# Kernel optimization log

Hardware: AMD Instinct MI355X
Metric: run time of the kernel (lower is better)

The kernel has to match this reference:

```python
import jax, jax.numpy as jnp
import numpy as np

N, E = 50000, 600000
IN_DIM, H, D = 256, 4, 128
NEG_SLOPE = 0.2


def setup_inputs() -> dict:
    key = jax.random.key(0)
    ks = jax.random.split(key, 9)
    x = jax.random.normal(ks[0], (N, IN_DIM), dtype=jnp.float32)
    src = jax.random.randint(ks[1], (E,), 0, N, dtype=jnp.int32)
    dst = jax.random.randint(ks[2], (E,), 0, N, dtype=jnp.int32)
    # layer 0: in=256 -> H*D=512; layer 1: in=H*D=512 -> H*D=512
    s0 = 1.0 / np.sqrt(IN_DIM)
    s1 = 1.0 / np.sqrt(H * D)
    W0 = jax.random.normal(ks[3], (IN_DIM, H * D), dtype=jnp.float32) * s0
    al0 = jax.random.normal(ks[4], (H, D), dtype=jnp.float32) * s1
    ar0 = jax.random.normal(ks[5], (H, D), dtype=jnp.float32) * s1
    W1 = jax.random.normal(ks[6], (H * D, H * D), dtype=jnp.float32) * s1
    al1 = jax.random.normal(ks[7], (H, D), dtype=jnp.float32) * s1
    ar1 = jax.random.normal(ks[8], (H, D), dtype=jnp.float32) * s1
    return {"x": x, "src": src, "dst": dst,
            "W0": W0, "al0": al0, "ar0": ar0,
            "W1": W1, "al1": al1, "ar1": ar1}


def gat_conv(x, W, al, ar, src, dst):
    """One DGL-style GATConv layer. x:[N,in] -> out:[N,H,D] (post relu)."""
    h = (x @ W).reshape(N, H, D)                       # fc, no bias
    el = jnp.sum(h * al, axis=-1)                      # [N,H]
    er = jnp.sum(h * ar, axis=-1)                      # [N,H]
    e = jax.nn.leaky_relu(el[src] + er[dst], NEG_SLOPE)  # [E,H]
    # edge softmax over incoming edges of each dst node (numerically stable)
    m = jax.ops.segment_max(e, dst, num_segments=N)    # [N,H]
    m = jnp.where(jnp.isfinite(m), m, 0.0)             # empty segments -> -inf
    ex = jnp.exp(e - m[dst])                           # [E,H]
    denom = jax.ops.segment_sum(ex, dst, num_segments=N)  # [N,H]
    alpha = ex / denom[dst]                            # [E,H]
    msg = alpha[:, :, None] * h[src]                   # [E,H,D]
    rst = jax.ops.segment_sum(msg, dst, num_segments=N)  # [N,H,D]
    return jax.nn.relu(rst)                            # activation=F.relu


def reference(x, src, dst, W0, al0, ar0, W1, al1, ar1):
    h = gat_conv(x, W0, al0, ar0, src, dst)            # [N,H,D]
    h = h.reshape(N, H * D)                            # flatten(1)
    h = gat_conv(h, W1, al1, ar1, src, dst)            # [N,H,D]
    return h.mean(axis=1)                              # mean over heads -> [N,D]
```

## Files before the change

kernel.cpp:

```cpp
#include <hip/hip_runtime.h>

#define NN 50000
#define NE 600000
#define DD 128
#define HD 512
#define NB 196

typedef unsigned short u16;
typedef __attribute__((ext_vector_type(8))) short short8;
typedef __attribute__((ext_vector_type(4))) float floatx4;

__device__ inline float b2f(u16 u) {
  return __uint_as_float(((unsigned int)u) << 16);
}
__device__ inline u16 f2b(float f) {
  unsigned int u = __float_as_uint(f);
  u = u + 0x7FFFu + ((u >> 16) & 1u);
  return (u16)(u >> 16);
}

__global__ void transpose_k(const float* __restrict__ W, u16* __restrict__ Wt, int K) {
  int idx = blockIdx.x * 256 + threadIdx.x;
  if (idx >= K * 512) return;
  int k = idx >> 9, n = idx & 511;
  Wt[n * K + k] = f2b(W[idx]);
}

__global__ void count_k(const int* __restrict__ dst, int* __restrict__ counts) {
  int e = blockIdx.x * 256 + threadIdx.x;
  if (e < NE) atomicAdd(&counts[dst[e]], 1);
}

__global__ __launch_bounds__(256) void blockscan_k(const int* __restrict__ counts,
                                                   int* __restrict__ rowp,
                                                   int* __restrict__ bsums) {
  __shared__ int tmp[256];
  int t = threadIdx.x;
  int i = blockIdx.x * 256 + t;
  int v = (i < NN) ? counts[i] : 0;
  tmp[t] = v;
  __syncthreads();
  for (int off = 1; off < 256; off <<= 1) {
    int u = (t >= off) ? tmp[t - off] : 0;
    __syncthreads();
    tmp[t] += u;
    __syncthreads();
  }
  if (i < NN) rowp[i] = tmp[t] - v;
  if (t == 255) bsums[blockIdx.x] = tmp[t];
}

__global__ __launch_bounds__(256) void bscan_k(const int* __restrict__ bsums,
                                               int* __restrict__ boffs) {
  __shared__ int tmp[256];
  int t = threadIdx.x;
  int v = (t < NB) ? bsums[t] : 0;
  tmp[t] = v;
  __syncthreads();
  for (int off = 1; off < 256; off <<= 1) {
    int u = (t >= off) ? tmp[t - off] : 0;
    __syncthreads();
    tmp[t] += u;
    __syncthreads();
  }
  if (t < NB) boffs[t] = tmp[t] - v;
}

__global__ void addoff_k(int* __restrict__ rowp, int* __restrict__ cursor,
                         const int* __restrict__ boffs) {
  int i = blockIdx.x * 256 + threadIdx.x;
  if (i < NN) {
    int v = rowp[i] + boffs[blockIdx.x];
    rowp[i] = v;
    cursor[i] = v;
  }
  if (i == 0) rowp[NN] = NE;
}

__global__ void scatter_k(const int* __restrict__ src, const int* __restrict__ dst,
                          int* __restrict__ cursor, int* __restrict__ csrs) {
  int e = blockIdx.x * 256 + threadIdx.x;
  if (e < NE) {
    int d = dst[e];
    int pos = atomicAdd(&cursor[d], 1);
    csrs[pos] = src[e];
  }
}

template <int K, bool A_F32>
__global__ __launch_bounds__(256) void gemm_el_er(
    const void* __restrict__ Ap, const u16* __restrict__ Wt,
    const float* __restrict__ al, const float* __restrict__ ar,
    u16* __restrict__ h, float* __restrict__ el, float* __restrict__ er) {
  constexpr int WS = 40;
  __shared__ u16 Wt_s[512 * WS];

  const int tid = threadIdx.x;
  const int w = tid >> 6, lane = tid & 63, quad = lane >> 4, l16 = lane & 15;
  const int rg = w >> 1, cg = w & 1;
  const int bm = blockIdx.x;

  floatx4 acc[16] = {};

  const int rowA = bm * 32 + rg * 16 + l16;
  const long arow = (rowA < NN) ? rowA : (NN - 1);

  const int sr0 = tid >> 2;
  const int sck = (tid & 3) * 8;

  for (int k0 = 0; k0 < K; k0 += 32) {
#pragma unroll
    for (int rr = 0; rr < 8; ++rr) {
      int r = sr0 + rr * 64;
      *(short8*)(Wt_s + r * WS + sck) =
          *(const short8*)(Wt + (long)r * K + k0 + sck);
    }
    __syncthreads();
    short8 af;
    if (A_F32) {
      const float* Af = (const float*)Ap;
      floatx4 v0 = *(const floatx4*)(Af + arow * K + k0 + quad * 8);
      floatx4 v1 = *(const floatx4*)(Af + arow * K + k0 + quad * 8 + 4);
      u16 tmp[8];
#pragma unroll
      for (int j = 0; j < 4; ++j) tmp[j] = f2b(v0[j]);
#pragma unroll
      for (int j = 0; j < 4; ++j) tmp[4 + j] = f2b(v1[j]);
      af = *(short8*)tmp;
    } else {
      af = *(const short8*)((const u16*)Ap + arow * K + k0 + quad * 8);
    }
#pragma unroll
    for (int ct = 0; ct < 16; ++ct) {
      short8 bf = *(const short8*)(Wt_s + (cg * 256 + ct * 16 + l16) * WS + quad * 8);
      acc[ct] = __builtin_amdgcn_mfma_f32_16x16x32_bf16(af, bf, acc[ct], 0, 0, 0);
    }
    __syncthreads();
  }

  float alv[16], arv[16];
#pragma unroll
  for (int ct = 0; ct < 16; ++ct) {
    int col = cg * 256 + ct * 16 + l16;
    alv[ct] = al[col];
    arv[ct] = ar[col];
  }
#pragma unroll
  for (int reg = 0; reg < 4; ++reg) {
    const int r = bm * 32 + rg * 16 + quad * 4 + reg;
    float pel[2] = {0.f, 0.f}, per_[2] = {0.f, 0.f};
#pragma unroll
    for (int ct = 0; ct < 16; ++ct) {
      int hh = ct >> 3;
      float v = acc[ct][reg];
      pel[hh] += v * alv[ct];
      per_[hh] += v * arv[ct];
    }
#pragma unroll
    for (int m = 1; m < 16; m <<= 1) {
      pel[0] += __shfl_xor(pel[0], m, 64);
      pel[1] += __shfl_xor(pel[1], m, 64);
      per_[0] += __shfl_xor(per_[0], m, 64);
      per_[1] += __shfl_xor(per_[1], m, 64);
    }
    if (r < NN) {
#pragma unroll
      for (int ct = 0; ct < 16; ++ct)
        h[(long)r * HD + cg * 256 + ct * 16 + l16] = f2b(acc[ct][reg]);
      if (l16 == 0) {
        el[r * 4 + cg * 2] = pel[0];
        el[r * 4 + cg * 2 + 1] = pel[1];
        er[r * 4 + cg * 2] = per_[0];
        er[r * 4 + cg * 2 + 1] = per_[1];
      }
    }
  }
}

template <int MODE>
__global__ __launch_bounds__(256) void aggregate(
    const u16* __restrict__ h, const float* __restrict__ el,
    const float* __restrict__ er, const int* __restrict__ rowp,
    const int* __restrict__ csrs, u16* __restrict__ ob, float* __restrict__ of) {
  const int wv = threadIdx.x >> 6, lane = threadIdx.x & 63;
  const int n = blockIdx.x * 4 + wv;
  if (n >= NN) return;
  const int base = rowp[n];
  const int deg = rowp[n + 1] - base;
  const int head = lane >> 4;

  if (deg == 0) {
    if (MODE == 0) {
      short8 z = {};
      *(short8*)(ob + (long)n * HD + lane * 8) = z;
    } else if (lane < 16) {
      floatx4 z = {};
      *(floatx4*)(of + (long)n * DD + lane * 8) = z;
      *(floatx4*)(of + (long)n * DD + lane * 8 + 4) = z;
    }
    return;
  }

  const floatx4 erv = *(const floatx4*)(er + n * 4);

  float mx[4] = {-1e30f, -1e30f, -1e30f, -1e30f};
  for (int i = lane; i < deg; i += 64) {
    int s = csrs[base + i];
    const floatx4 ev = *(const floatx4*)(el + s * 4);
#pragma unroll
    for (int hh = 0; hh < 4; ++hh) {
      float e = ev[hh] + erv[hh];
      e = (e > 0.f) ? e : 0.2f * e;
      mx[hh] = fmaxf(mx[hh], e);
    }
  }
#pragma unroll
  for (int hh = 0; hh < 4; ++hh)
#pragma unroll
    for (int m = 1; m < 64; m <<= 1) mx[hh] = fmaxf(mx[hh], __shfl_xor(mx[hh], m, 64));

  float sm[4] = {0.f, 0.f, 0.f, 0.f};
  for (int i = lane; i < deg; i += 64) {
    int s = csrs[base + i];
    const floatx4 ev = *(const floatx4*)(el + s * 4);
#pragma unroll
    for (int hh = 0; hh < 4; ++hh) {
      float e = ev[hh] + erv[hh];
      e = (e > 0.f) ? e : 0.2f * e;
      sm[hh] += __expf(e - mx[hh]);
    }
  }
#pragma unroll
  for (int hh = 0; hh < 4; ++hh)
#pragma unroll
    for (int m = 1; m < 64; m <<= 1) sm[hh] += __shfl_xor(sm[hh], m, 64);

  const float m_h = mx[head];
  const float inv_h = 1.f / sm[head];
  const float er_h = erv[head];

  float acc[8] = {0.f, 0.f, 0.f, 0.f, 0.f, 0.f, 0.f, 0.f};
  int i = 0;
  for (; i + 4 <= deg; i += 4) {
    int s0 = csrs[base + i], s1 = csrs[base + i + 1];
    int s2 = csrs[base + i + 2], s3 = csrs[base + i + 3];
    const short8 hv0 = *(const short8*)(h + (long)s0 * HD + lane * 8);
    const short8 hv1 = *(const short8*)(h + (long)s1 * HD + lane * 8);
    const short8 hv2 = *(const short8*)(h + (long)s2 * HD + lane * 8);
    const short8 hv3 = *(const short8*)(h + (long)s3 * HD + lane * 8);
    float e0 = el[s0 * 4 + head] + er_h;
    float e1 = el[s1 * 4 + head] + er_h;
    float e2 = el[s2 * 4 + head] + er_h;
    float e3 = el[s3 * 4 + head] + er_h;
    e0 = (e0 > 0.f) ? e0 : 0.2f * e0;
    e1 = (e1 > 0.f) ? e1 : 0.2f * e1;
    e2 = (e2 > 0.f) ? e2 : 0.2f * e2;
    e3 = (e3 > 0.f) ? e3 : 0.2f * e3;
    float w0 = __expf(e0 - m_h) * inv_h;
    float w1 = __expf(e1 - m_h) * inv_h;
    float w2 = __expf(e2 - m_h) * inv_h;
    float w3 = __expf(e3 - m_h) * inv_h;
#pragma unroll
    for (int j = 0; j < 8; ++j) acc[j] += w0 * b2f((u16)hv0[j]);
#pragma unroll
    for (int j = 0; j < 8; ++j) acc[j] += w1 * b2f((u16)hv1[j]);
#pragma unroll
    for (int j = 0; j < 8; ++j) acc[j] += w2 * b2f((u16)hv2[j]);
#pragma unroll
    for (int j = 0; j < 8; ++j) acc[j] += w3 * b2f((u16)hv3[j]);
  }
  for (; i < deg; ++i) {
    int s = csrs[base + i];
    float e = el[s * 4 + head] + er_h;
    const short8 hv = *(const short8*)(h + (long)s * HD + lane * 8);
    e = (e > 0.f) ? e : 0.2f * e;
    float wgt = __expf(e - m_h) * inv_h;
#pragma unroll
    for (int j = 0; j < 8; ++j) acc[j] += wgt * b2f((u16)hv[j]);
  }

#pragma unroll
  for (int j = 0; j < 8; ++j) acc[j] = fmaxf(acc[j], 0.f);

  if (MODE == 0) {
    u16 ub[8];
#pragma unroll
    for (int j = 0; j < 8; ++j) ub[j] = f2b(acc[j]);
    *(short8*)(ob + (long)n * HD + lane * 8) = *(short8*)ub;
  } else {
#pragma unroll
    for (int j = 0; j < 8; ++j) acc[j] += __shfl_xor(acc[j], 16, 64);
#pragma unroll
    for (int j = 0; j < 8; ++j) acc[j] += __shfl_xor(acc[j], 32, 64);
    if (lane < 16) {
      floatx4 o0, o1;
#pragma unroll
      for (int j = 0; j < 4; ++j) o0[j] = acc[j] * 0.25f;
#pragma unroll
      for (int j = 0; j < 4; ++j) o1[j] = acc[4 + j] * 0.25f;
      *(floatx4*)(of + (long)n * DD + lane * 8) = o0;
      *(floatx4*)(of + (long)n * DD + lane * 8 + 4) = o1;
    }
  }
}

extern "C" void kernel_launch(void* const* d_in, const int* in_sizes, int n_in,
                              void* d_out, int out_size, void* d_ws, size_t ws_size,
                              hipStream_t stream) {
  const float* x = (const float*)d_in[0];
  const int* src = (const int*)d_in[1];
  const int* dst = (const int*)d_in[2];
  const float* W0 = (const float*)d_in[3];
  const float* al0 = (const float*)d_in[4];
  const float* ar0 = (const float*)d_in[5];
  const float* W1 = (const float*)d_in[6];
  const float* al1 = (const float*)d_in[7];
  const float* ar1 = (const float*)d_in[8];
  float* out = (float*)d_out;

  char* p = (char*)d_ws;
  u16* h = (u16*)p;        p += (size_t)NN * HD * 2;
  u16* rst0 = (u16*)p;     p += (size_t)NN * HD * 2;
  float* el = (float*)p;   p += (size_t)NN * 4 * 4;
  float* er = (float*)p;   p += (size_t)NN * 4 * 4;
  u16* Wt0 = (u16*)p;      p += 512 * 256 * 2;
  u16* Wt1 = (u16*)p;      p += 512 * 512 * 2;
  int* counts = (int*)p;   p += (size_t)NN * 4;
  int* cursor = (int*)p;   p += (size_t)NN * 4;
  int* rowp = (int*)p;     p += (size_t)(NN + 1) * 4;
  int* bsums = (int*)p;    p += 256 * 4;
  int* boffs = (int*)p;    p += 256 * 4;
  int* csrs = (int*)p;     p += (size_t)NE * 4;

  hipMemsetAsync(counts, 0, NN * sizeof(int), stream);
  count_k<<<(NE + 255) / 256, 256, 0, stream>>>(dst, counts);
  blockscan_k<<<NB, 256, 0, stream>>>(counts, rowp, bsums);
  bscan_k<<<1, 256, 0, stream>>>(bsums, boffs);
  addoff_k<<<NB, 256, 0, stream>>>(rowp, cursor, boffs);
  scatter_k<<<(NE + 255) / 256, 256, 0, stream>>>(src, dst, cursor, csrs);
  transpose_k<<<(256 * 512 + 255) / 256, 256, 0, stream>>>(W0, Wt0, 256);
  transpose_k<<<(512 * 512 + 255) / 256, 256, 0, stream>>>(W1, Wt1, 512);

  const int gblocks = (NN + 31) / 32;
  gemm_el_er<256, true><<<gblocks, 256, 0, stream>>>(x, Wt0, al0, ar0, h, el, er);
  aggregate<0><<<(NN + 3) / 4, 256, 0, stream>>>(h, el, er, rowp, csrs, rst0, nullptr);
  gemm_el_er<512, false><<<gblocks, 256, 0, stream>>>(rst0, Wt1, al1, ar1, h, el, er);
  aggregate<1><<<(NN + 3) / 4, 256, 0, stream>>>(h, el, er, rowp, csrs, nullptr, out);
}
```

Before: 560.1 us.

## Drop softmax max pass, double GEMM row tile, replace memset with kernel

The aggregate kernel no longer runs the two pre-passes that compute the per-head max and the softmax denominator. It accumulates unnormalized exp weights and their sum in the main gather loop and normalizes once at the end. This removes two extra passes over the edge list and el gathers, but drops the max subtraction, so large logits could overflow. The GEMM now computes 64 rows per block instead of 32, reusing each LDS-staged W tile for twice as many MFMAs at the cost of more accumulator registers. The counts memset is replaced by a small zeroing kernel.

```diff
diff --git a/kernel.cpp b/kernel.cpp
--- a/kernel.cpp
+++ b/kernel.cpp
@@ -17,6 +17,11 @@
   unsigned int u = __float_as_uint(f);
   u = u + 0x7FFFu + ((u >> 16) & 1u);
   return (u16)(u >> 16);
+}
+
+__global__ void zero_k(int* __restrict__ p, int n) {
+  int i = blockIdx.x * 256 + threadIdx.x;
+  if (i < n) p[i] = 0;
 }
 
 __global__ void transpose_k(const float* __restrict__ W, u16* __restrict__ Wt, int K) {
@@ -100,10 +105,14 @@
   const int rg = w >> 1, cg = w & 1;
   const int bm = blockIdx.x;
 
-  floatx4 acc[16] = {};
-
-  const int rowA = bm * 32 + rg * 16 + l16;
-  const long arow = (rowA < NN) ? rowA : (NN - 1);
+  floatx4 acc[2][16] = {};
+
+  long arow[2];
+#pragma unroll
+  for (int a = 0; a < 2; ++a) {
+    int rowA = bm * 64 + rg * 32 + a * 16 + l16;
+    arow[a] = (rowA < NN) ? rowA : (NN - 1);
+  }
 
   const int sr0 = tid >> 2;
   const int sck = (tid & 3) * 8;
@@ -116,24 +125,28 @@
           *(const short8*)(Wt + (long)r * K + k0 + sck);
     }
     __syncthreads();
-    short8 af;
-    if (A_F32) {
-      const float* Af = (const float*)Ap;
-      floatx4 v0 = *(const floatx4*)(Af + arow * K + k0 + quad * 8);
-      floatx4 v1 = *(const floatx4*)(Af + arow * K + k0 + quad * 8 + 4);
-      u16 tmp[8];
-#pragma unroll
-      for (int j = 0; j < 4; ++j) tmp[j] = f2b(v0[j]);
-#pragma unroll
-      for (int j = 0; j < 4; ++j) tmp[4 + j] = f2b(v1[j]);
-      af = *(short8*)tmp;
-    } else {
-      af = *(const short8*)((const u16*)Ap + arow * K + k0 + quad * 8);
+    short8 af[2];
+#pragma unroll
+    for (int a = 0; a < 2; ++a) {
+      if (A_F32) {
+        const float* Af = (const float*)Ap;
+        floatx4 v0 = *(const floatx4*)(Af + arow[a] * K + k0 + quad * 8);
+        floatx4 v1 = *(const floatx4*)(Af + arow[a] * K + k0 + quad * 8 + 4);
+        u16 tmp[8];
+#pragma unroll
+        for (int j = 0; j < 4; ++j) tmp[j] = f2b(v0[j]);
+#pragma unroll
+        for (int j = 0; j < 4; ++j) tmp[4 + j] = f2b(v1[j]);
+        af[a] = *(short8*)tmp;
+      } else {
+        af[a] = *(const short8*)((const u16*)Ap + arow[a] * K + k0 + quad * 8);
+      }
     }
 #pragma unroll
     for (int ct = 0; ct < 16; ++ct) {
       short8 bf = *(const short8*)(Wt_s + (cg * 256 + ct * 16 + l16) * WS + quad * 8);
-      acc[ct] = __builtin_amdgcn_mfma_f32_16x16x32_bf16(af, bf, acc[ct], 0, 0, 0);
+      acc[0][ct] = __builtin_amdgcn_mfma_f32_16x16x32_bf16(af[0], bf, acc[0][ct], 0, 0, 0);
+      acc[1][ct] = __builtin_amdgcn_mfma_f32_16x16x32_bf16(af[1], bf, acc[1][ct], 0, 0, 0);
     }
     __syncthreads();
   }
@@ -146,32 +159,35 @@
     arv[ct] = ar[col];
   }
 #pragma unroll
-  for (int reg = 0; reg < 4; ++reg) {
-    const int r = bm * 32 + rg * 16 + quad * 4 + reg;
-    float pel[2] = {0.f, 0.f}, per_[2] = {0.f, 0.f};
-#pragma unroll
-    for (int ct = 0; ct < 16; ++ct) {
-      int hh = ct >> 3;
-      float v = acc[ct][reg];
-      pel[hh] += v * alv[ct];
-      per_[hh] += v * arv[ct];
-    }
-#pragma unroll
-    for (int m = 1; m < 16; m <<= 1) {
-      pel[0] += __shfl_xor(pel[0], m, 64);
-      pel[1] += __shfl_xor(pel[1], m, 64);
-      per_[0] += __shfl_xor(per_[0], m, 64);
-      per_[1] += __shfl_xor(per_[1], m, 64);
-    }
-    if (r < NN) {
-#pragma unroll
-      for (int ct = 0; ct < 16; ++ct)
-        h[(long)r * HD + cg * 256 + ct * 16 + l16] = f2b(acc[ct][reg]);
-      if (l16 == 0) {
-        el[r * 4 + cg * 2] = pel[0];
-        el[r * 4 + cg * 2 + 1] = pel[1];
-        er[r * 4 + cg * 2] = per_[0];
-        er[r * 4 + cg * 2 + 1] = per_[1];
+  for (int a = 0; a < 2; ++a) {
+#pragma unroll
+    for (int reg = 0; reg < 4; ++reg) {
+      const int r = bm * 64 + rg * 32 + a * 16 + quad * 4 + reg;
+      float pel[2] = {0.f, 0.f}, per_[2] = {0.f, 0.f};
+#pragma unroll
+      for (int ct = 0; ct < 16; ++ct) {
+        int hh = ct >> 3;
+        float v = acc[a][ct][reg];
+        pel[hh] += v * alv[ct];
+        per_[hh] += v * arv[ct];
+      }
+#pragma unroll
+      for (int m = 1; m < 16; m <<= 1) {
+        pel[0] += __shfl_xor(pel[0], m, 64);
+        pel[1] += __shfl_xor(pel[1], m, 64);
+        per_[0] += __shfl_xor(per_[0], m, 64);
+        per_[1] += __shfl_xor(per_[1], m, 64);
+      }
+      if (r < NN) {
+#pragma unroll
+        for (int ct = 0; ct < 16; ++ct)
+          h[(long)r * HD + cg * 256 + ct * 16 + l16] = f2b(acc[a][ct][reg]);
+        if (l16 == 0) {
+          el[r * 4 + cg * 2] = pel[0];
+          el[r * 4 + cg * 2 + 1] = pel[1];
+          er[r * 4 + cg * 2] = per_[0];
+          er[r * 4 + cg * 2 + 1] = per_[1];
+        }
       }
     }
   }
@@ -201,45 +217,10 @@
     return;
   }
 
-  const floatx4 erv = *(const floatx4*)(er + n * 4);
-
-  float mx[4] = {-1e30f, -1e30f, -1e30f, -1e30f};
-  for (int i = lane; i < deg; i += 64) {
-    int s = csrs[base + i];
-    const floatx4 ev = *(const floatx4*)(el + s * 4);
-#pragma unroll
-    for (int hh = 0; hh < 4; ++hh) {
-      float e = ev[hh] + erv[hh];
-      e = (e > 0.f) ? e : 0.2f * e;
-      mx[hh] = fmaxf(mx[hh], e);
-    }
-  }
-#pragma unroll
-  for (int hh = 0; hh < 4; ++hh)
-#pragma unroll
-    for (int m = 1; m < 64; m <<= 1) mx[hh] = fmaxf(mx[hh], __shfl_xor(mx[hh], m, 64));
-
-  float sm[4] = {0.f, 0.f, 0.f, 0.f};
-  for (int i = lane; i < deg; i += 64) {
-    int s = csrs[base + i];
-    const floatx4 ev = *(const floatx4*)(el + s * 4);
-#pragma unroll
-    for (int hh = 0; hh < 4; ++hh) {
-      float e = ev[hh] + erv[hh];
-      e = (e > 0.f) ? e : 0.2f * e;
-      sm[hh] += __expf(e - mx[hh]);
-    }
-  }
-#pragma unroll
-  for (int hh = 0; hh < 4; ++hh)
-#pragma unroll
-    for (int m = 1; m < 64; m <<= 1) sm[hh] += __shfl_xor(sm[hh], m, 64);
-
-  const float m_h = mx[head];
-  const float inv_h = 1.f / sm[head];
-  const float er_h = erv[head];
+  const float er_h = er[n * 4 + head];
 
   float acc[8] = {0.f, 0.f, 0.f, 0.f, 0.f, 0.f, 0.f, 0.f};
+  float sm = 0.f;
   int i = 0;
   for (; i + 4 <= deg; i += 4) {
     int s0 = csrs[base + i], s1 = csrs[base + i + 1];
@@ -256,10 +237,11 @@
     e1 = (e1 > 0.f) ? e1 : 0.2f * e1;
     e2 = (e2 > 0.f) ? e2 : 0.2f * e2;
     e3 = (e3 > 0.f) ? e3 : 0.2f * e3;
-    float w0 = __expf(e0 - m_h) * inv_h;
-    float w1 = __expf(e1 - m_h) * inv_h;
-    float w2 = __expf(e2 - m_h) * inv_h;
-    float w3 = __expf(e3 - m_h) * inv_h;
+    float w0 = __expf(e0);
+    float w1 = __expf(e1);
+    float w2 = __expf(e2);
+    float w3 = __expf(e3);
+    sm += (w0 + w1) + (w2 + w3);
 #pragma unroll
     for (int j = 0; j < 8; ++j) acc[j] += w0 * b2f((u16)hv0[j]);
 #pragma unroll
@@ -274,13 +256,15 @@
     float e = el[s * 4 + head] + er_h;
     const short8 hv = *(const short8*)(h + (long)s * HD + lane * 8);
     e = (e > 0.f) ? e : 0.2f * e;
-    float wgt = __expf(e - m_h) * inv_h;
+    float wgt = __expf(e);
+    sm += wgt;
 #pragma unroll
     for (int j = 0; j < 8; ++j) acc[j] += wgt * b2f((u16)hv[j]);
   }
 
-#pragma unroll
-  for (int j = 0; j < 8; ++j) acc[j] = fmaxf(acc[j], 0.f);
+  const float inv = 1.f / sm;
+#pragma unroll
+  for (int j = 0; j < 8; ++j) acc[j] = fmaxf(acc[j] * inv, 0.f);
 
   if (MODE == 0) {
     u16 ub[8];
@@ -332,7 +316,7 @@
   int* boffs = (int*)p;    p += 256 * 4;
   int* csrs = (int*)p;     p += (size_t)NE * 4;
 
-  hipMemsetAsync(counts, 0, NN * sizeof(int), stream);
+  zero_k<<<NB, 256, 0, stream>>>(counts, NN);
   count_k<<<(NE + 255) / 256, 256, 0, stream>>>(dst, counts);
   blockscan_k<<<NB, 256, 0, stream>>>(counts, rowp, bsums);
   bscan_k<<<1, 256, 0, stream>>>(bsums, boffs);
@@ -341,7 +325,7 @@
   transpose_k<<<(256 * 512 + 255) / 256, 256, 0, stream>>>(W0, Wt0, 256);
   transpose_k<<<(512 * 512 + 255) / 256, 256, 0, stream>>>(W1, Wt1, 512);
 
-  const int gblocks = (NN + 31) / 32;
+  const int gblocks = (NN + 63) / 64;
   gemm_el_er<256, true><<<gblocks, 256, 0, stream>>>(x, Wt0, al0, ar0, h, el, er);
   aggregate<0><<<(NN + 3) / 4, 256, 0, stream>>>(h, el, er, rowp, csrs, rst0, nullptr);
   gemm_el_er<512, false><<<gblocks, 256, 0, stream>>>(rst0, Wt1, al1, ar1, h, el, er);
```

Result: no change. 551.4 us (-1.6%).
